# Kernel optimization log

Hardware: AMD Instinct MI355X
Metric: run time of the kernel (lower is better)

The kernel has to match this reference:

```python
import jax, jax.numpy as jnp
import numpy as np

NUM_BLOCKS = 32
B, S = 8, 2048


def setup_inputs() -> dict:
    key = jax.random.key(0)
    k1, k2, k3 = jax.random.split(key, 3)
    h = jax.random.uniform(k1, (B, S, NUM_BLOCKS, 4), dtype=jnp.float32)
    W = jax.random.uniform(k2, (B, S, NUM_BLOCKS, NUM_BLOCKS), dtype=jnp.float32)
    stim = jax.random.uniform(k3, (B, S, NUM_BLOCKS), dtype=jnp.float32)
    return {"h": h, "W": W, "stim": stim}


def _step(h, W, stim):
    nb = h.shape[-2]
    eye = jnp.eye(nb, dtype=W.dtype)
    W_no_self = W * (1.0 - eye)                      # zero self-connections
    # neighbor inflow: [b,s,i,j] @ [b,s,j,c] -> [b,s,i,c]
    inflow = jnp.einsum('bsij,bsjc->bsic', W_no_self, h)
    total_w = W_no_self.sum(axis=-1, keepdims=True) + 1e-8
    neigh = inflow / total_w                          # weighted neighbor mean

    E, P, G, L = h[..., 0], h[..., 1], h[..., 2], h[..., 3]
    En, Pn, Gn, Ln = neigh[..., 0], neigh[..., 1], neigh[..., 2], neigh[..., 3]

    clamp01 = lambda x: jnp.clip(x, 0.0, 1.0)
    E_new = clamp01(E + 0.3 * stim - 0.4 * P - 0.2 * G)
    P_new = clamp01(P + 0.5 * stim + 0.3 * (Pn - P) - 0.2 * E)
    G_new = clamp01(G + 0.4 * E * (1.0 - P) + 0.2 * (Gn - G) - 0.3 * P)
    good_neighbor = 0.5 * En + 0.5 * Gn
    L_new = clamp01(L + 0.4 * good_neighbor + 0.3 * (Ln - L) - 0.3 * P)

    h_new = jnp.stack([E_new, P_new, G_new, L_new], axis=-1)  # [b,s,nb,4]

    # pairwise euclidean distance over the 4 EPGL channels (torch.cdist p=2)
    diff = h_new[..., :, None, :] - h_new[..., None, :, :]    # [b,s,nb,nb,4]
    sq = jnp.sum(diff * diff, axis=-1)
    # safe sqrt: zero distance -> 0 (matches cdist; avoids nan grads)
    h_diff = jnp.where(sq > 0, jnp.sqrt(jnp.where(sq > 0, sq, 1.0)), 0.0)

    mutual_L = 0.5 * (L_new[..., :, None] + L_new[..., None, :])
    alpha, beta = 0.1 * mutual_L, 0.05
    W_new = W + alpha * h_diff - beta * W
    W_new = jnp.clip(W_new, 0.0, 1.0) * (1.0 - eye)
    return h_new, W_new


def reference(h, W, stim):
    return _step(h, W, stim)
```

## Files before the change

### kernel.cpp

```cpp
#include <hip/hip_runtime.h>

#define NB 32
#define WAVES_PER_BLOCK 4

typedef float nfloat4 __attribute__((ext_vector_type(4)));

__device__ __forceinline__ void nt_store4(const float4& v, float4* p) {
    __builtin_nontemporal_store(*(const nfloat4*)&v, (nfloat4*)p);
}

__device__ __forceinline__ float clamp01(float x) {
    return fminf(fmaxf(x, 0.0f), 1.0f);
}

__global__ __launch_bounds__(256, 6) void biotoken_step(
    const float* __restrict__ h,
    const float* __restrict__ W,
    const float* __restrict__ stim,
    float* __restrict__ out_h,
    float* __restrict__ out_W)
{
    const int lw    = threadIdx.x & 63;
    const int wave  = threadIdx.x >> 6;
    const int token = blockIdx.x * WAVES_PER_BLOCK + wave;
    const int i     = lw & 31;
    const int half  = lw >> 5;

    __shared__ float s_hin [WAVES_PER_BLOCK][NB * 4];
    __shared__ float s_hnew[WAVES_PER_BLOCK][NB * 4];
    __shared__ float s_W   [WAVES_PER_BLOCK][NB * 33];

    const float4* Wt = (const float4*)(W + (size_t)token * (NB * NB));
    const float4* ht = (const float4*)(h + (size_t)token * (NB * 4));

    float4 wr[4];
    wr[0] = Wt[0 * 64 + lw];
    wr[1] = Wt[1 * 64 + lw];
    wr[2] = Wt[2 * 64 + lw];
    wr[3] = Wt[3 * 64 + lw];
    const float sti = stim[(size_t)token * NB + i];

    if (lw < NB) {
        ((float4*)s_hin[wave])[lw] = ht[lw];
    }

    {
        float* sw = s_W[wave];
        const int g = lw >> 3;
        const int c = (lw & 7) * 4;
        #pragma unroll
        for (int k = 0; k < 4; ++k) {
            const int r = k * 8 + g;
            const float* wp = (const float*)&wr[k];
            sw[r * 33 + c + 0] = wp[0];
            sw[r * 33 + c + 1] = wp[1];
            sw[r * 33 + c + 2] = wp[2];
            sw[r * 33 + c + 3] = wp[3];
        }
    }
    __builtin_amdgcn_wave_barrier();

    const float* sw   = s_W[wave];
    const float* shin = s_hin[wave];

    float accE = 0.f, accP = 0.f, accG = 0.f, accL = 0.f, tot = 0.f;
    #pragma unroll
    for (int t = 0; t < 16; ++t) {
        const int j = half * 16 + t;
        float w = sw[i * 33 + j];
        w = (j == i) ? 0.0f : w;
        const float4 hj = *(const float4*)&shin[j * 4];
        accE = fmaf(w, hj.x, accE);
        accP = fmaf(w, hj.y, accP);
        accG = fmaf(w, hj.z, accG);
        accL = fmaf(w, hj.w, accL);
        tot += w;
    }
    accE += __shfl_xor(accE, 32);
    accP += __shfl_xor(accP, 32);
    accG += __shfl_xor(accG, 32);
    accL += __shfl_xor(accL, 32);
    tot  += __shfl_xor(tot,  32);

    const float inv = 1.0f / (tot + 1e-8f);
    const float En = accE * inv, Pn = accP * inv, Gn = accG * inv, Ln = accL * inv;

    const float4 hi = *(const float4*)&shin[i * 4];
    const float E = hi.x, P = hi.y, G = hi.z, L = hi.w;

    const float E_new = clamp01(E + 0.3f * sti - 0.4f * P - 0.2f * G);
    const float P_new = clamp01(P + 0.5f * sti + 0.3f * (Pn - P) - 0.2f * E);
    const float G_new = clamp01(G + 0.4f * E * (1.0f - P) + 0.2f * (Gn - G) - 0.3f * P);
    const float good  = 0.5f * En + 0.5f * Gn;
    const float L_new = clamp01(L + 0.4f * good + 0.3f * (Ln - L) - 0.3f * P);

    if (half == 0) {
        const float4 hn = make_float4(E_new, P_new, G_new, L_new);
        ((float4*)s_hnew[wave])[i] = hn;
        nt_store4(hn, &((float4*)(out_h + (size_t)token * (NB * 4)))[i]);
    }
    __builtin_amdgcn_wave_barrier();

    const float* shn = s_hnew[wave];
    float4* outWt = (float4*)(out_W + (size_t)token * (NB * NB));

    const int jb0 = (lw & 7) * 4;
    float4 hjv[4];
    #pragma unroll
    for (int e = 0; e < 4; ++e) {
        hjv[e] = *(const float4*)&shn[(jb0 + e) * 4];
    }

    #pragma unroll
    for (int k = 0; k < 4; ++k) {
        const int m  = k * 64 + lw;
        const int r  = m >> 3;
        const float4 hr = *(const float4*)&shn[r * 4];
        const float  Lr = hr.w;
        const float* wp = (const float*)&wr[k];
        float4 res;
        float* resp = &res.x;
        #pragma unroll
        for (int e = 0; e < 4; ++e) {
            const int j = jb0 + e;
            const float4 hj = hjv[e];
            const float dx = hr.x - hj.x;
            const float dy = hr.y - hj.y;
            const float dz = hr.z - hj.z;
            const float dw = hr.w - hj.w;
            const float sq = dx * dx + dy * dy + dz * dz + dw * dw;
            const float dist = sqrtf(sq);
            const float mutual = 0.5f * (Lr + hj.w);
            float wn = 0.95f * wp[e] + 0.1f * mutual * dist;
            wn = clamp01(wn);
            resp[e] = (j == r) ? 0.0f : wn;
        }
        nt_store4(res, &outWt[m]);
    }
}

extern "C" void kernel_launch(void* const* d_in, const int* in_sizes, int n_in,
                              void* d_out, int out_size, void* d_ws, size_t ws_size,
                              hipStream_t stream) {
    const float* h    = (const float*)d_in[0];
    const float* W    = (const float*)d_in[1];
    const float* stim = (const float*)d_in[2];

    const int tokens = in_sizes[2] / NB;
    float* out_h = (float*)d_out;
    float* out_W = (float*)d_out + (size_t)tokens * NB * 4;

    const int blocks = tokens / WAVES_PER_BLOCK;
    biotoken_step<<<blocks, 256, 0, stream>>>(h, W, stim, out_h, out_W);
}
```

Measured before the change: 136.8 us.

## Load W rows directly per lane, drop LDS transpose and nontemporal stores

Each lane now loads the 16 contiguous W entries it needs for its row (i, half) straight into registers, which removes the shared-memory staging of W and its bank-padded transpose. The output W row segment is computed from those same registers, and the row's h_new comes from the lane's own registers, not from LDS. Nontemporal stores become plain stores and the occupancy hint rises from 6 to 8. The cost is that global loads and stores are now strided by 128 bytes across lanes instead of fully coalesced, which may cut memory efficiency.

```diff
diff --git a/kernel.cpp b/kernel.cpp
--- a/kernel.cpp
+++ b/kernel.cpp
@@ -3,17 +3,11 @@
 #define NB 32
 #define WAVES_PER_BLOCK 4
 
-typedef float nfloat4 __attribute__((ext_vector_type(4)));
-
-__device__ __forceinline__ void nt_store4(const float4& v, float4* p) {
-    __builtin_nontemporal_store(*(const nfloat4*)&v, (nfloat4*)p);
-}
-
 __device__ __forceinline__ float clamp01(float x) {
     return fminf(fmaxf(x, 0.0f), 1.0f);
 }
 
-__global__ __launch_bounds__(256, 6) void biotoken_step(
+__global__ __launch_bounds__(256, 8) void biotoken_step(
     const float* __restrict__ h,
     const float* __restrict__ W,
     const float* __restrict__ stim,
@@ -25,49 +19,34 @@
     const int token = blockIdx.x * WAVES_PER_BLOCK + wave;
     const int i     = lw & 31;
     const int half  = lw >> 5;
+    const int c0    = half * 16;
 
     __shared__ float s_hin [WAVES_PER_BLOCK][NB * 4];
     __shared__ float s_hnew[WAVES_PER_BLOCK][NB * 4];
-    __shared__ float s_W   [WAVES_PER_BLOCK][NB * 33];
 
-    const float4* Wt = (const float4*)(W + (size_t)token * (NB * NB));
-    const float4* ht = (const float4*)(h + (size_t)token * (NB * 4));
-
-    float4 wr[4];
-    wr[0] = Wt[0 * 64 + lw];
-    wr[1] = Wt[1 * 64 + lw];
-    wr[2] = Wt[2 * 64 + lw];
-    wr[3] = Wt[3 * 64 + lw];
-    const float sti = stim[(size_t)token * NB + i];
+    const float*  Wt  = W + (size_t)token * (NB * NB);
+    const float4* wrp = (const float4*)(Wt + i * NB + c0);
+    float4 wrow[4];
+    wrow[0] = wrp[0];
+    wrow[1] = wrp[1];
+    wrow[2] = wrp[2];
+    wrow[3] = wrp[3];
 
     if (lw < NB) {
-        ((float4*)s_hin[wave])[lw] = ht[lw];
+        ((float4*)s_hin[wave])[lw] =
+            ((const float4*)(h + (size_t)token * (NB * 4)))[lw];
     }
-
-    {
-        float* sw = s_W[wave];
-        const int g = lw >> 3;
-        const int c = (lw & 7) * 4;
-        #pragma unroll
-        for (int k = 0; k < 4; ++k) {
-            const int r = k * 8 + g;
-            const float* wp = (const float*)&wr[k];
-            sw[r * 33 + c + 0] = wp[0];
-            sw[r * 33 + c + 1] = wp[1];
-            sw[r * 33 + c + 2] = wp[2];
-            sw[r * 33 + c + 3] = wp[3];
-        }
-    }
+    const float sti = stim[(size_t)token * NB + i];
     __builtin_amdgcn_wave_barrier();
 
-    const float* sw   = s_W[wave];
     const float* shin = s_hin[wave];
+    const float* wf   = (const float*)wrow;
 
     float accE = 0.f, accP = 0.f, accG = 0.f, accL = 0.f, tot = 0.f;
     #pragma unroll
     for (int t = 0; t < 16; ++t) {
-        const int j = half * 16 + t;
-        float w = sw[i * 33 + j];
+        const int j = c0 + t;
+        float w = wf[t];
         w = (j == i) ? 0.0f : w;
         const float4 hj = *(const float4*)&shin[j * 4];
         accE = fmaf(w, hj.x, accE);
@@ -94,36 +73,26 @@
     const float good  = 0.5f * En + 0.5f * Gn;
     const float L_new = clamp01(L + 0.4f * good + 0.3f * (Ln - L) - 0.3f * P);
 
+    const float4 hr = make_float4(E_new, P_new, G_new, L_new);
     if (half == 0) {
-        const float4 hn = make_float4(E_new, P_new, G_new, L_new);
-        ((float4*)s_hnew[wave])[i] = hn;
-        nt_store4(hn, &((float4*)(out_h + (size_t)token * (NB * 4)))[i]);
+        ((float4*)s_hnew[wave])[i] = hr;
+        ((float4*)(out_h + (size_t)token * (NB * 4)))[i] = hr;
     }
     __builtin_amdgcn_wave_barrier();
 
     const float* shn = s_hnew[wave];
-    float4* outWt = (float4*)(out_W + (size_t)token * (NB * NB));
+    const float  Lr  = hr.w;
+    float4* outWr = (float4*)(out_W + (size_t)token * (NB * NB) + i * NB + c0);
 
-    const int jb0 = (lw & 7) * 4;
-    float4 hjv[4];
     #pragma unroll
     for (int e = 0; e < 4; ++e) {
-        hjv[e] = *(const float4*)&shn[(jb0 + e) * 4];
-    }
-
-    #pragma unroll
-    for (int k = 0; k < 4; ++k) {
-        const int m  = k * 64 + lw;
-        const int r  = m >> 3;
-        const float4 hr = *(const float4*)&shn[r * 4];
-        const float  Lr = hr.w;
-        const float* wp = (const float*)&wr[k];
         float4 res;
         float* resp = &res.x;
         #pragma unroll
-        for (int e = 0; e < 4; ++e) {
-            const int j = jb0 + e;
-            const float4 hj = hjv[e];
+        for (int q = 0; q < 4; ++q) {
+            const int t = 4 * e + q;
+            const int j = c0 + t;
+            const float4 hj = *(const float4*)&shn[j * 4];
             const float dx = hr.x - hj.x;
             const float dy = hr.y - hj.y;
             const float dz = hr.z - hj.z;
@@ -131,11 +100,11 @@
             const float sq = dx * dx + dy * dy + dz * dz + dw * dw;
             const float dist = sqrtf(sq);
             const float mutual = 0.5f * (Lr + hj.w);
-            float wn = 0.95f * wp[e] + 0.1f * mutual * dist;
+            float wn = 0.95f * wf[t] + 0.1f * mutual * dist;
             wn = clamp01(wn);
-            resp[e] = (j == r) ? 0.0f : wn;
+            resp[q] = (j == i) ? 0.0f : wn;
         }
-        nt_store4(res, &outWt[m]);
+        outWr[e] = res;
     }
 }
 
```

New measurement: 142.9 us. 4.5% more time.
